# Performance work log

Measured on AMD Instinct MI355X. Metric: run time of the kernel, lower is better.

The kernel has to match this reference:

```python
import jax, jax.numpy as jnp
import numpy as np
from jax import lax
from jax.scipy.special import logsumexp

N, M, K = 50000, 1024, 64          # points, nodes, points-per-patch
D_PT, D_NODE = 64, 256             # point / node feature dims
NUM_CORR = 256                     # coarse correspondences (OT batch)
FINE_TOPK = 3
CONF_TH = 0.05
OUT_CORR = 1024                    # fixed-size fine correspondence output
OT_ITERS = 100
NEG = -1e4                         # finite stand-in for -inf (grad-safe)
EPS = 1e-8


def setup_inputs() -> dict:
    key = jax.random.key(0)
    k = jax.random.split(key, 13)
    f = jnp.float32
    return {
        "src_points": jax.random.uniform(k[0], (N, 3), f) * 10.0,
        "tgt_points": jax.random.uniform(k[1], (N, 3), f) * 10.0,
        "src_point_feats": jax.random.normal(k[2], (N, D_PT), f),
        "tgt_point_feats": jax.random.normal(k[3], (N, D_PT), f),
        "src_node_feats": jax.random.normal(k[4], (M, D_NODE), f),
        "tgt_node_feats": jax.random.normal(k[5], (M, D_NODE), f),
        "src_node_xyz": jax.random.uniform(k[6], (M, 3), f) * 10.0,
        "tgt_node_xyz": jax.random.uniform(k[7], (M, 3), f) * 10.0,
        "coarse_w": jax.random.normal(k[8], (D_NODE, D_NODE), f) / np.sqrt(D_NODE),
        "coarse_b": jnp.zeros((D_NODE,), f),
        "fine_w": jax.random.normal(k[9], (D_NODE, D_PT), f) / np.sqrt(D_PT),
        "fine_b": jnp.zeros((D_NODE,), f),
        "alpha": jnp.ones((), f),
    }


def sq_dist(a, b):
    # squared pairwise distance via gram trick, (Na, Nb)
    return (jnp.sum(a * a, -1)[:, None] + jnp.sum(b * b, -1)[None, :]
            - 2.0 * a @ b.T)


def point_to_node_partition(points, nodes):
    d = sq_dist(points, nodes)                       # (N, M)
    p2n = jnp.argmin(d, axis=1)                      # nearest node per point
    m = nodes.shape[0]
    node_masks = jnp.zeros((m,), bool).at[p2n].set(True)
    match = p2n[:, None] == jnp.arange(m)[None, :]   # point assigned to node
    dm = jnp.where(match, d, 1e12)
    _, knn_idx = lax.top_k(-dm.T, K)                 # (M, K) nearest assigned pts
    knn_node = p2n[knn_idx]
    knn_masks = knn_node == jnp.arange(m)[:, None]
    knn_idx = jnp.where(knn_masks, knn_idx, points.shape[0])  # pad index = N
    return node_masks, knn_idx, knn_masks


def coarse_matching(tgt_feats, src_feats, tgt_masks, src_masks):
    # exp(-||.||^2) similarity + dual normalization (GeoTransformer style)
    scores = jnp.exp(-sq_dist(tgt_feats, src_feats))
    valid = tgt_masks[:, None] & src_masks[None, :]
    scores = jnp.where(valid, scores, 0.0)
    s = (scores / (scores.sum(1, keepdims=True) + EPS)) * \
        (scores / (scores.sum(0, keepdims=True) + EPS))
    vals, idx = lax.top_k(s.reshape(-1), NUM_CORR)
    tgt_idx = idx // src_feats.shape[0]
    src_idx = idx % src_feats.shape[0]
    return tgt_idx, src_idx, vals


def log_optimal_transport(scores, row_masks, col_masks, alpha):
    B, R, C = scores.shape
    pad_c = jnp.broadcast_to(alpha, (B, R, 1)).astype(scores.dtype)
    pad_r = jnp.broadcast_to(alpha, (B, 1, C + 1)).astype(scores.dtype)
    padded = jnp.concatenate([jnp.concatenate([scores, pad_c], 2), pad_r], 1)
    inv_r = jnp.concatenate([~row_masks, jnp.zeros((B, 1), bool)], 1)  # (B,R+1)
    inv_c = jnp.concatenate([~col_masks, jnp.zeros((B, 1), bool)], 1)  # (B,C+1)
    padded = jnp.where(inv_r[:, :, None] | inv_c[:, None, :], NEG, padded)
    nr = row_masks.sum(1).astype(scores.dtype)
    nc = col_masks.sum(1).astype(scores.dtype)
    norm = -jnp.log(nr + nc)
    log_mu = jnp.concatenate(
        [jnp.broadcast_to(norm[:, None], (B, R)), (jnp.log(nc) + norm)[:, None]], 1)
    log_mu = jnp.where(inv_r, NEG, log_mu)
    log_nu = jnp.concatenate(
        [jnp.broadcast_to(norm[:, None], (B, C)), (jnp.log(nr) + norm)[:, None]], 1)
    log_nu = jnp.where(inv_c, NEG, log_nu)

    def body(_, uv):
        u, v = uv
        u = log_mu - logsumexp(padded + v[:, None, :], axis=2)
        v = log_nu - logsumexp(padded + u[:, :, None], axis=1)
        return (u, v)

    u, v = lax.fori_loop(0, OT_ITERS, body,
                         (jnp.zeros_like(log_mu), jnp.zeros_like(log_nu)))
    return padded + u[:, :, None] + v[:, None, :] - norm[:, None, None]


def _topk_row_mask(s, k):
    # boolean mask: True where s is among top-k along the last axis
    idx = lax.top_k(s, k)[1]                          # (B, R, k)
    B, R, _ = s.shape
    b = jnp.arange(B)[:, None, None]
    r = jnp.arange(R)[None, :, None]
    return jnp.zeros(s.shape, bool).at[b, r, idx].set(True)


def fine_matching(tgt_knn_pts, src_knn_pts, tgt_masks, src_masks, ot_scores):
    s = jnp.exp(ot_scores[:, :K, :K])                 # drop dustbin
    mask = tgt_masks[:, :, None] & src_masks[:, None, :]
    rm = _topk_row_mask(s, FINE_TOPK)
    cm = jnp.swapaxes(_topk_row_mask(jnp.swapaxes(s, 1, 2), FINE_TOPK), 1, 2)
    corr = rm & cm & (s > CONF_TH) & mask             # mutual topk + threshold
    sm = jnp.where(corr, s, 0.0)
    vals, idx = lax.top_k(sm.reshape(-1), OUT_CORR)   # fixed-size extraction
    b = idx // (K * K)
    r = (idx // K) % K
    c = idx % K
    valid = vals > 0.0
    tp = jnp.where(valid[:, None], tgt_knn_pts[b, r], 0.0)
    sp = jnp.where(valid[:, None], src_knn_pts[b, c], 0.0)
    return tp, sp, jnp.where(valid, vals, 0.0)


def reference(src_points, tgt_points, src_point_feats, tgt_point_feats,
              src_node_feats, tgt_node_feats, src_node_xyz, tgt_node_xyz,
              coarse_w, coarse_b, fine_w, fine_b, alpha):
    def l2n(x):
        return x / jnp.linalg.norm(x, axis=1, keepdims=True)

    s_node_f = l2n(src_node_feats @ coarse_w.T + coarse_b)
    t_node_f = l2n(tgt_node_feats @ coarse_w.T + coarse_b)
    s_pt_f = src_point_feats @ fine_w.T + fine_b       # (N, 256)
    t_pt_f = tgt_point_feats @ fine_w.T + fine_b

    s_nm, s_knn_i, s_knn_m = point_to_node_partition(src_points, src_node_xyz)
    t_nm, t_knn_i, t_knn_m = point_to_node_partition(tgt_points, tgt_node_xyz)

    s_pad_pts = jnp.concatenate([src_points, jnp.zeros((1, 3), src_points.dtype)], 0)
    t_pad_pts = jnp.concatenate([tgt_points, jnp.zeros((1, 3), tgt_points.dtype)], 0)
    s_knn_pts = s_pad_pts[s_knn_i]                     # (M, K, 3)
    t_knn_pts = t_pad_pts[t_knn_i]

    # coarse matching is under no_grad in the original
    t_ci, s_ci, node_scores = coarse_matching(
        lax.stop_gradient(t_node_f), lax.stop_gradient(s_node_f), t_nm, s_nm)

    s_c_knn_i = s_knn_i[s_ci]; t_c_knn_i = t_knn_i[t_ci]     # (B, K)
    s_c_knn_m = s_knn_m[s_ci]; t_c_knn_m = t_knn_m[t_ci]
    s_c_knn_p = s_knn_pts[s_ci]; t_c_knn_p = t_knn_pts[t_ci]  # (B, K, 3)

    s_pad_f = jnp.concatenate([s_pt_f, jnp.zeros((1, D_NODE), s_pt_f.dtype)], 0)
    t_pad_f = jnp.concatenate([t_pt_f, jnp.zeros((1, D_NODE), t_pt_f.dtype)], 0)
    s_c_knn_f = s_pad_f[s_c_knn_i]                     # (B, K, 256)
    t_c_knn_f = t_pad_f[t_c_knn_i]

    ms = jnp.einsum('bnd,bmd->bnm', t_c_knn_f, s_c_knn_f) / jnp.sqrt(
        jnp.asarray(D_NODE, t_c_knn_f.dtype))
    ms = log_optimal_transport(ms, t_c_knn_m, s_c_knn_m, alpha)  # (B, K+1, K+1)

    tp, sp, cs = fine_matching(lax.stop_gradient(t_c_knn_p),
                               lax.stop_gradient(s_c_knn_p),
                               t_c_knn_m, s_c_knn_m, lax.stop_gradient(ms))
    return ms, tp, sp, cs
```

## Files before the change

### kernel.cpp

```cpp
#include <hip/hip_runtime.h>
#include <math.h>

#define NPTS 50000
#define MN 1024
#define KK 64
#define DPT 64
#define DN 256
#define BCORR 256
#define OUTC 1024
#define OTI 100
#define NEGV (-1e4f)
#define EPSV 1e-8f
#define CAPL 512
#define CCAP 16384
#define HBLK 256
#define RCH 2048

__global__ void zero_all_kernel(int* cnt_s, int* cnt_t, int* ci_t, int* ci_s,
                                float* tpout){
  int t=blockIdx.x*256+threadIdx.x;
  if (t<MN){ cnt_s[t]=0; cnt_t[t]=0; }
  if (t<BCORR){ ci_t[t]=0; ci_s[t]=0; }
  for (int i=t;i<OUTC*3*2+OUTC;i+=gridDim.x*256) tpout[i]=0.0f;
}

__device__ __forceinline__ float blockReduceSum256(float v, float* red){
  int t=threadIdx.x;
  red[t]=v; __syncthreads();
  #pragma unroll
  for (int s=128;s>0;s>>=1){ if(t<s) red[t]+=red[t+s]; __syncthreads(); }
  float r=red[0]; __syncthreads();
  return r;
}

__device__ __forceinline__ void hist_add_agg(unsigned* lh, bool act, unsigned bkt){
  unsigned long long ma=__ballot(act);
  if (ma==0ULL) return;
  unsigned b0=__shfl(bkt, 0, 64);
  unsigned long long m=__ballot(act && bkt==b0);
  int lane=threadIdx.x&63;
  if (m==ma){
    int leader=__ffsll((long long)ma)-1;
    if (act && lane==leader) atomicAdd(&lh[b0],(unsigned)__popcll(ma));
  } else if (act){
    atomicAdd(&lh[bkt],1u);
  }
}

__global__ __launch_bounds__(256) void node_gemm_kernel(
    const float* __restrict__ xt, const float* __restrict__ xs_,
    const float* __restrict__ W, const float* __restrict__ bias,
    float* __restrict__ raw){
  __shared__ float Xs[64][64];
  __shared__ float Ws[64][64];
  int bi=blockIdx.x>>2, bo=blockIdx.x&3;
  const float* x=(bi<16)? xt:xs_;
  int rowbase=(bi&15)*64;
  int t=threadIdx.x, r=t&63, kq=t>>6, tx=t&15, ty=t>>4;
  float acc[4][4]={};
  for (int kc=0;kc<DN;kc+=64){
    __syncthreads();
    const float* xr=x+(size_t)(rowbase+r)*DN+kc+kq*16;
    const float* wr=W+(size_t)(bo*64+r)*DN+kc+kq*16;
    #pragma unroll
    for (int j4=0;j4<4;j4++){
      float4 v=*(const float4*)(xr+4*j4);
      Xs[kq*16+4*j4+0][r]=v.x; Xs[kq*16+4*j4+1][r]=v.y;
      Xs[kq*16+4*j4+2][r]=v.z; Xs[kq*16+4*j4+3][r]=v.w;
      float4 w=*(const float4*)(wr+4*j4);
      Ws[kq*16+4*j4+0][r]=w.x; Ws[kq*16+4*j4+1][r]=w.y;
      Ws[kq*16+4*j4+2][r]=w.z; Ws[kq*16+4*j4+3][r]=w.w;
    }
    __syncthreads();
    #pragma unroll
    for (int kk=0;kk<64;kk++){
      float4 a4=*(const float4*)(&Xs[kk][4*ty]);
      float4 w4=*(const float4*)(&Ws[kk][4*tx]);
      float av[4]={a4.x,a4.y,a4.z,a4.w};
      float wv[4]={w4.x,w4.y,w4.z,w4.w};
      #pragma unroll
      for (int i=0;i<4;i++)
        #pragma unroll
        for (int j=0;j<4;j++) acc[i][j]=fmaf(av[i],wv[j],acc[i][j]);
    }
  }
  size_t gr=(size_t)(bi*64)*DN;
  #pragma unroll
  for (int i=0;i<4;i++){
    int rr=4*ty+i;
    #pragma unroll
    for (int j=0;j<4;j++){
      int oo=4*tx+j;
      raw[gr+(size_t)rr*DN+bo*64+oo]=acc[i][j]+bias[bo*64+oo];
    }
  }
}
__global__ __launch_bounds__(256) void node_norm_kernel(
    const float* __restrict__ raw,
    float* __restrict__ outt, float* __restrict__ outs,
    float* __restrict__ sqt, float* __restrict__ sqs){
  __shared__ float red[256];
  int m=blockIdx.x, i=threadIdx.x;
  float* out=(m<MN)? outt:outs;
  float* sq=(m<MN)? sqt:sqs;
  int mm=(m<MN)? m:m-MN;
  float acc=raw[(size_t)m*DN+i];
  float ssq=blockReduceSum256(acc*acc,red);
  float o=acc/sqrtf(ssq);
  out[mm*DN+i]=o;
  float s2=blockReduceSum256(o*o,red);
  if(i==0) sq[mm]=s2;
}

__global__ __launch_bounds__(256) void p2n_scatter_kernel(
    const float* __restrict__ pts_s, const float* __restrict__ nd_s,
    int* __restrict__ c_s, int* __restrict__ l_s,
    const float* __restrict__ pts_t, const float* __restrict__ nd_t,
    int* __restrict__ c_t, int* __restrict__ l_t,
    int pb){
  __shared__ __align__(16) float4 nd[MN];
  int which=blockIdx.x>=pb;
  const float* pts=which? pts_t:pts_s;
  const float* nodes=which? nd_t:nd_s;
  int* cnt=which? c_t:c_s;
  int* list=which? l_t:l_s;
  int blk=which? blockIdx.x-pb : blockIdx.x;
  for (int j=threadIdx.x;j<MN;j+=256){
    float a=nodes[j*3+0], b=nodes[j*3+1], c=nodes[j*3+2];
    nd[j]=make_float4(a,b,c,a*a+b*b+c*c);
  }
  __syncthreads();
  int id=blk*256+threadIdx.x;
  if (id>=NPTS) return;
  float px=pts[id*3+0], py=pts[id*3+1], pz=pts[id*3+2];
  float pp=px*px+py*py+pz*pz;
  float best=3.4e38f; int bi=0;
  for (int j=0;j<MN;j++){
    float4 n=nd[j];
    float d=pp+n.w-2.0f*(px*n.x+py*n.y+pz*n.z);
    if (d<best){best=d;bi=j;}
  }
  int slot=atomicAdd(&cnt[bi],1);
  if (slot<CAPL) list[(size_t)bi*CAPL+slot]=id;
}

__global__ __launch_bounds__(256) void knn_kernel(
    const float* __restrict__ pts_s, const float* __restrict__ nd_s,
    const int* __restrict__ c_s, const int* __restrict__ l_s, int* __restrict__ k_s,
    const float* __restrict__ pts_t, const float* __restrict__ nd_t,
    const int* __restrict__ c_t, const int* __restrict__ l_t, int* __restrict__ k_t){
  __shared__ float ds[CAPL];
  __shared__ int is[CAPL];
  int which=blockIdx.x>=MN;
  const float* pts=which? pts_t:pts_s;
  const float* nodes=which? nd_t:nd_s;
  const int* cnt=which? c_t:c_s;
  const int* list=which? l_t:l_s;
  int* knn=which? k_t:k_s;
  int m=which? blockIdx.x-MN : blockIdx.x;
  int c=cnt[m]; if (c>CAPL) c=CAPL;
  float ax=nodes[m*3+0], ay=nodes[m*3+1], az=nodes[m*3+2];
  float nn2=ax*ax+ay*ay+az*az;
  for (int e=threadIdx.x;e<c;e+=256){
    int p=list[(size_t)m*CAPL+e];
    float px=pts[p*3+0],py=pts[p*3+1],pz=pts[p*3+2];
    float pp=px*px+py*py+pz*pz;
    ds[e]=pp+nn2-2.0f*(px*ax+py*ay+pz*az);
    is[e]=p;
  }
  for (int k=threadIdx.x;k<KK;k+=256) knn[m*KK+k]=NPTS;
  __syncthreads();
  for (int e=threadIdx.x;e<c;e+=256){
    float d=ds[e]; int p=is[e]; int r=0;
    for (int j=0;j<c;j++){
      float dj=ds[j];
      r += (dj<d || (dj==d && is[j]<p)) ? 1 : 0;
    }
    if (r<KK) knn[m*KK+r]=p;
  }
}

__global__ __launch_bounds__(256) void coarse_score_kernel(
    const float* __restrict__ tf, const float* __restrict__ sf,
    const float* __restrict__ tt, const float* __restrict__ ssv,
    const int* __restrict__ cnt_t, const int* __restrict__ cnt_s, float* __restrict__ S){
  __shared__ float tas[64][64];
  __shared__ float sbs[64][64];
  __shared__ float tta[64], ssa[64], tva[64], sva[64];
  int bi=blockIdx.x>>4, bj=blockIdx.x&15;
  int t=threadIdx.x, r=t&63, kq=t>>6, tx=t&15, ty=t>>4;
  if (kq==0){ tta[r]=tt[bi*64+r]; tva[r]=(cnt_t[bi*64+r]>0)?1.f:0.f; }
  if (kq==1){ ssa[r]=ssv[bj*64+r]; sva[r]=(cnt_s[bj*64+r]>0)?1.f:0.f; }
  float acc[4][4]={};
  const float* ta=tf+((size_t)bi*64)*DN;
  const float* sa=sf+((size_t)bj*64)*DN;
  for (int kc=0;kc<DN;kc+=64){
    __syncthreads();
    const float* tr_=ta+(size_t)r*DN+kc+kq*16;
    const float* sr_=sa+(size_t)r*DN+kc+kq*16;
    #pragma unroll
    for (int j4=0;j4<4;j4++){
      float4 v=*(const float4*)(tr_+4*j4);
      tas[kq*16+4*j4+0][r]=v.x; tas[kq*16+4*j4+1][r]=v.y;
      tas[kq*16+4*j4+2][r]=v.z; tas[kq*16+4*j4+3][r]=v.w;
      float4 w=*(const float4*)(sr_+4*j4);
      sbs[kq*16+4*j4+0][r]=w.x; sbs[kq*16+4*j4+1][r]=w.y;
      sbs[kq*16+4*j4+2][r]=w.z; sbs[kq*16+4*j4+3][r]=w.w;
    }
    __syncthreads();
    #pragma unroll
    for (int kk=0;kk<64;kk++){
      float4 a4=*(const float4*)(&tas[kk][4*ty]);
      float4 b4=*(const float4*)(&sbs[kk][4*tx]);
      float av[4]={a4.x,a4.y,a4.z,a4.w};
      float bv[4]={b4.x,b4.y,b4.z,b4.w};
      #pragma unroll
      for (int i=0;i<4;i++)
        #pragma unroll
        for (int j=0;j<4;j++) acc[i][j]=fmaf(av[i],bv[j],acc[i][j]);
    }
  }
  __syncthreads();
  #pragma unroll
  for (int i=0;i<4;i++){
    int rr=4*ty+i;
    #pragma unroll
    for (int j=0;j<4;j++){
      int cc=4*tx+j;
      float d=tta[rr]+ssa[cc]-2.0f*acc[i][j];
      float v=expf(-d);
      S[(size_t)(bi*64+rr)*MN + bj*64+cc]=(tva[rr]>0.f && sva[cc]>0.f)? v:0.0f;
    }
  }
}

__global__ __launch_bounds__(256) void sums_kernel(
    const float* __restrict__ S, float* __restrict__ rs, float* __restrict__ cs){
  __shared__ float red[256];
  __shared__ float red2[16][17];
  if (blockIdx.x<MN){
    int i=blockIdx.x;
    float a=0;
    for (int j=threadIdx.x;j<MN;j+=256) a+=S[(size_t)i*MN+j];
    float r=blockReduceSum256(a,red);
    if (threadIdx.x==0) rs[i]=r;
  } else {
    int j0=(blockIdx.x-MN)*16;
    int tx=threadIdx.x&15, ty=threadIdx.x>>4;
    float a=0;
    for (int i=ty;i<MN;i+=16) a+=S[(size_t)i*MN + j0+tx];
    red2[ty][tx]=a; __syncthreads();
    if (ty==0){
      float s=0;
      #pragma unroll
      for (int q=0;q<16;q++) s+=red2[q][tx];
      cs[j0+tx]=s;
    }
  }
}
__global__ __launch_bounds__(256) void dualnorm_hist_kernel(
    float* __restrict__ S, const float* __restrict__ rs, const float* __restrict__ cs,
    unsigned* __restrict__ partial1){
  __shared__ unsigned lh[256];
  lh[threadIdx.x]=0u; __syncthreads();
  for (int idx=blockIdx.x*256+threadIdx.x; idx<MN*MN; idx+=gridDim.x*256){
    int i=idx>>10, j=idx&1023;
    float v=S[idx];
    v=(v/(rs[i]+EPSV))*(v/(cs[j]+EPSV));
    S[idx]=v;
    bool act=(v>0.0f);
    unsigned bkt=act? (__float_as_uint(v)>>24) : 0xFFFFFFFFu;
    hist_add_agg(lh,act,bkt);
  }
  __syncthreads();
  partial1[blockIdx.x*256+threadIdx.x]=lh[threadIdx.x];
}

__device__ __forceinline__ int scan_top(const unsigned* h, int k, unsigned start,
                                        unsigned* outcum){
  unsigned cum=start;
  for (int b=255;b>=0;b--){
    if (cum+h[b] >= (unsigned)k){ *outcum=cum; return b; }
    cum+=h[b];
  }
  *outcum=cum;
  return -1;
}
__device__ __forceinline__ void sum_partials(const unsigned* __restrict__ p,
                                             unsigned* h, int t){
  unsigned a=0;
  for (int i=0;i<HBLK;i++) a+=p[(size_t)i*256+t];
  h[t]=a;
}

__global__ __launch_bounds__(256) void hist_fine_kernel(
    const float* __restrict__ arr, int n, int k,
    const unsigned* __restrict__ p1, unsigned* __restrict__ p2){
  __shared__ unsigned h[256];
  __shared__ unsigned lh[256];
  __shared__ unsigned cbS;
  int t=threadIdx.x;
  lh[t]=0u;
  sum_partials(p1,h,t);
  __syncthreads();
  if (t==0){
    unsigned ab; int cb=scan_top(h,k,0u,&ab);
    if (cb<0) cb=0;
    cbS=(unsigned)cb;
  }
  __syncthreads();
  unsigned CB=cbS;
  for (int i=blockIdx.x*256+t; i<n; i+=gridDim.x*256){
    float v=arr[i];
    unsigned b=__float_as_uint(v);
    bool act=(v>0.0f && (b>>24)==CB);
    hist_add_agg(lh,act,(b>>16)&255u);
  }
  __syncthreads();
  p2[blockIdx.x*256+t]=lh[t];
}
__global__ __launch_bounds__(256) void hist_fine2_kernel(
    const float* __restrict__ arr, int n, int k,
    const unsigned* __restrict__ p1, const unsigned* __restrict__ p2,
    unsigned* __restrict__ p3, unsigned* __restrict__ cnt){
  __shared__ unsigned h[256];
  __shared__ unsigned lh[256];
  __shared__ unsigned t16S;
  int t=threadIdx.x;
  if (blockIdx.x==0 && t==0) *cnt=0u;
  lh[t]=0u;
  sum_partials(p1,h,t);
  __syncthreads();
  __shared__ unsigned cbS, ab1S;
  if (t==0){
    unsigned ab; int cb=scan_top(h,k,0u,&ab);
    if (cb<0){ cb=0; ab=ab-h[0]; }
    cbS=(unsigned)cb; ab1S=ab;
  }
  __syncthreads();
  sum_partials(p2,h,t);
  __syncthreads();
  if (t==0){
    unsigned ab2; int sb=scan_top(h,k,ab1S,&ab2);
    if (sb<0) sb=0;
    t16S=cbS*256u+(unsigned)sb;
  }
  __syncthreads();
  unsigned T16=t16S;
  for (int i=blockIdx.x*256+t; i<n; i+=gridDim.x*256){
    float v=arr[i];
    unsigned b=__float_as_uint(v);
    bool act=(v>0.0f && (b>>16)==T16);
    hist_add_agg(lh,act,(b>>8)&255u);
  }
  __syncthreads();
  p3[blockIdx.x*256+t]=lh[t];
}
__global__ __launch_bounds__(256) void compact_kernel(
    const float* __restrict__ arr, int n, int k,
    const unsigned* __restrict__ p1, const unsigned* __restrict__ p2,
    const unsigned* __restrict__ p3,
    float* __restrict__ cv, int* __restrict__ ci, unsigned* __restrict__ cnt){
  __shared__ unsigned h[256];
  __shared__ unsigned cbS, ab1S, t16S, ab2S, t24S;
  int t=threadIdx.x;
  sum_partials(p1,h,t);
  __syncthreads();
  if (t==0){
    unsigned ab; int cb=scan_top(h,k,0u,&ab);
    if (cb<0){ cb=0; ab=ab-h[0]; }
    cbS=(unsigned)cb; ab1S=ab;
  }
  __syncthreads();
  sum_partials(p2,h,t);
  __syncthreads();
  if (t==0){
    unsigned ab2; int sb=scan_top(h,k,ab1S,&ab2);
    if (sb<0) sb=0;
    t16S=cbS*256u+(unsigned)sb; ab2S=ab2;
  }
  __syncthreads();
  sum_partials(p3,h,t);
  __syncthreads();
  if (t==0){
    unsigned ab3; int sb=scan_top(h,k,ab2S,&ab3);
    if (sb<0) sb=0;
    t24S=t16S*256u+(unsigned)sb;
  }
  __syncthreads();
  unsigned T=t24S;
  for (int i=blockIdx.x*256+t; i<n; i+=gridDim.x*256){
    float v=arr[i];
    if (v>0.0f && (__float_as_uint(v)>>8)>=T){
      unsigned p=atomicAdd(cnt,1u);
      if (p<CCAP){ cv[p]=v; ci[p]=i; }
    }
  }
}
__global__ __launch_bounds__(256) void rank_coarse_kernel(
    const float* __restrict__ cv, const int* __restrict__ ci, const unsigned* __restrict__ meta,
    int* __restrict__ ti, int* __restrict__ si){
  __shared__ __align__(16) float scv[RCH];
  __shared__ __align__(16) int sci[RCH];
  int c=(int)meta[1]; if (c>CCAP) c=CCAP;
  int t=blockIdx.x*256+threadIdx.x;
  bool act=(t<c);
  float v=0.0f; int idx=0;
  if (act){ v=cv[t]; idx=ci[t]; }
  int rk=0;
  for (int base=0;base<c;base+=RCH){
    int lim=min(RCH,c-base);
    __syncthreads();
    for (int j=threadIdx.x;j<lim;j+=256){ scv[j]=cv[base+j]; sci[j]=ci[base+j]; }
    __syncthreads();
    if (act){
      int j=0;
      for (;j+4<=lim;j+=4){
        float4 v4=*(const float4*)(scv+j);
        int4 i4=*(const int4*)(sci+j);
        rk += (v4.x>v||(v4.x==v&&i4.x<idx))?1:0;
        rk += (v4.y>v||(v4.y==v&&i4.y<idx))?1:0;
        rk += (v4.z>v||(v4.z==v&&i4.z<idx))?1:0;
        rk += (v4.w>v||(v4.w==v&&i4.w<idx))?1:0;
      }
      for (;j<lim;j++) rk += (scv[j]>v||(scv[j]==v&&sci[j]<idx))?1:0;
    }
  }
  if (act && rk<BCORR){ ti[rk]=idx/MN; si[rk]=idx%MN; }
}
__global__ __launch_bounds__(256) void rank_fine_kernel(
    const float* __restrict__ cv, const int* __restrict__ ci, const unsigned* __restrict__ meta,
    const int* __restrict__ sel_t, const int* __restrict__ sel_s,
    const float* __restrict__ tpts, const float* __restrict__ spts,
    float* __restrict__ tp, float* __restrict__ sp, float* __restrict__ cs){
  __shared__ __align__(16) float scv[RCH];
  __shared__ __align__(16) int sci[RCH];
  int c=(int)meta[1]; if (c>CCAP) c=CCAP;
  int t=blockIdx.x*256+threadIdx.x;
  bool act=(t<c);
  float v=0.0f; int idx=0;
  if (act){ v=cv[t]; idx=ci[t]; }
  int rk=0;
  for (int base=0;base<c;base+=RCH){
    int lim=min(RCH,c-base);
    __syncthreads();
    for (int j=threadIdx.x;j<lim;j+=256){ scv[j]=cv[base+j]; sci[j]=ci[base+j]; }
    __syncthreads();
    if (act){
      int j=0;
      for (;j+4<=lim;j+=4){
        float4 v4=*(const float4*)(scv+j);
        int4 i4=*(const int4*)(sci+j);
        rk += (v4.x>v||(v4.x==v&&i4.x<idx))?1:0;
        rk += (v4.y>v||(v4.y==v&&i4.y<idx))?1:0;
        rk += (v4.z>v||(v4.z==v&&i4.z<idx))?1:0;
        rk += (v4.w>v||(v4.w==v&&i4.w<idx))?1:0;
      }
      for (;j<lim;j++) rk += (scv[j]>v||(scv[j]==v&&sci[j]<idx))?1:0;
    }
  }
  if (act && rk<OUTC){
    int b=idx>>12, r=(idx>>6)&63, cc=idx&63;
    int tpi=sel_t[b*KK+r], spi=sel_s[b*KK+cc];
    float tx=0,ty=0,tz=0,sx=0,sy=0,sz=0;
    if (tpi<NPTS){ tx=tpts[tpi*3]; ty=tpts[tpi*3+1]; tz=tpts[tpi*3+2]; }
    if (spi<NPTS){ sx=spts[spi*3]; sy=spts[spi*3+1]; sz=spts[spi*3+2]; }
    tp[rk*3+0]=tx; tp[rk*3+1]=ty; tp[rk*3+2]=tz;
    sp[rk*3+0]=sx; sp[rk*3+1]=sy; sp[rk*3+2]=sz;
    cs[rk]=v;
  }
}

__global__ __launch_bounds__(256) void sel_feat_kernel(
    const int* __restrict__ ci_t, const int* __restrict__ knn_t, const float* __restrict__ ptf_t,
    const int* __restrict__ ci_s, const int* __restrict__ knn_s, const float* __restrict__ ptf_s,
    const float* __restrict__ W, const float* __restrict__ bias,
    float* __restrict__ out_t, float* __restrict__ out_s,
    int* __restrict__ sel_tO, int* __restrict__ sel_sO){
  __shared__ float Xs[64][64];
  __shared__ float Ws[64][64];
  __shared__ float pvf[64];
  int which=blockIdx.x>=1024;
  const int* cib=which? ci_s:ci_t;
  const int* knn=which? knn_s:knn_t;
  const float* ptf=which? ptf_s:ptf_t;
  float* out=which? out_s:out_t;
  int* sel=which? sel_sO:sel_tO;
  int blk=which? blockIdx.x-1024 : blockIdx.x;
  int bj=blk>>2, bo=blk&3;
  int t=threadIdx.x, r=t&63, kq=t>>6, tx=t&15, ty=t>>4;
  int p=knn[cib[bj]*KK+r];
  if (kq==0){
    pvf[r]=(p!=NPTS)?1.f:0.f;
    if (bo==0) sel[bj*KK+r]=p;
  }
  const float* xr=ptf+(size_t)p*DPT+kq*16;
  #pragma unroll
  for (int j4=0;j4<4;j4++){
    float4 v=(p==NPTS)? make_float4(0.f,0.f,0.f,0.f) : *(const float4*)(xr+4*j4);
    Xs[kq*16+4*j4+0][r]=v.x; Xs[kq*16+4*j4+1][r]=v.y;
    Xs[kq*16+4*j4+2][r]=v.z; Xs[kq*16+4*j4+3][r]=v.w;
  }
  const float* wr=W+(size_t)(bo*64+r)*DPT+kq*16;
  #pragma unroll
  for (int j4=0;j4<4;j4++){
    float4 w=*(const float4*)(wr+4*j4);
    Ws[kq*16+4*j4+0][r]=w.x; Ws[kq*16+4*j4+1][r]=w.y;
    Ws[kq*16+4*j4+2][r]=w.z; Ws[kq*16+4*j4+3][r]=w.w;
  }
  __syncthreads();
  float acc[4][4]={};
  #pragma unroll
  for (int kk=0;kk<64;kk++){
    float4 a4=*(const float4*)(&Xs[kk][4*ty]);
    float4 w4=*(const float4*)(&Ws[kk][4*tx]);
    float av[4]={a4.x,a4.y,a4.z,a4.w};
    float wv[4]={w4.x,w4.y,w4.z,w4.w};
    #pragma unroll
    for (int i=0;i<4;i++)
      #pragma unroll
      for (int j=0;j<4;j++) acc[i][j]=fmaf(av[i],wv[j],acc[i][j]);
  }
  #pragma unroll
  for (int i=0;i<4;i++){
    int rr=4*ty+i;
    #pragma unroll
    for (int j=0;j<4;j++){
      int oo=4*tx+j;
      float v=acc[i][j]+bias[bo*64+oo];
      out[(size_t)(bj*64+rr)*DN + bo*64+oo]= (pvf[rr]>0.f)? v : 0.0f;
    }
  }
}

__global__ __launch_bounds__(256) void pbuild_kernel(
    const float* __restrict__ ft, const float* __restrict__ fs,
    const int* __restrict__ sel_t, const int* __restrict__ sel_s,
    const float* __restrict__ alpha_p, float* __restrict__ P){
  __shared__ float tas[64][64];
  __shared__ float sbs[64][64];
  __shared__ float tmv[64], smv[64];
  int b=blockIdx.x, t=threadIdx.x;
  int r=t&63, kq=t>>6, tx=t&15, ty=t>>4;
  if (kq==0) tmv[r]=(sel_t[b*KK+r]!=NPTS)?1.f:0.f;
  if (kq==1) smv[r]=(sel_s[b*KK+r]!=NPTS)?1.f:0.f;
  float acc[4][4]={};
  const float* tb=ft+(size_t)b*KK*DN;
  const float* sb=fs+(size_t)b*KK*DN;
  for (int kc=0;kc<DN;kc+=64){
    __syncthreads();
    const float* tr_=tb+(size_t)r*DN+kc+kq*16;
    const float* sr_=sb+(size_t)r*DN+kc+kq*16;
    #pragma unroll
    for (int j4=0;j4<4;j4++){
      float4 v=*(const float4*)(tr_+4*j4);
      tas[kq*16+4*j4+0][r]=v.x; tas[kq*16+4*j4+1][r]=v.y;
      tas[kq*16+4*j4+2][r]=v.z; tas[kq*16+4*j4+3][r]=v.w;
      float4 w=*(const float4*)(sr_+4*j4);
      sbs[kq*16+4*j4+0][r]=w.x; sbs[kq*16+4*j4+1][r]=w.y;
      sbs[kq*16+4*j4+2][r]=w.z; sbs[kq*16+4*j4+3][r]=w.w;
    }
    __syncthreads();
    #pragma unroll
    for (int kk=0;kk<64;kk++){
      float4 a4=*(const float4*)(&tas[kk][4*ty]);
      float4 b4=*(const float4*)(&sbs[kk][4*tx]);
      float av[4]={a4.x,a4.y,a4.z,a4.w};
      float bv[4]={b4.x,b4.y,b4.z,b4.w};
      #pragma unroll
      for (int i=0;i<4;i++)
        #pragma unroll
        for (int j=0;j<4;j++) acc[i][j]=fmaf(av[i],bv[j],acc[i][j]);
    }
  }
  __syncthreads();
  float alpha=alpha_p[0];
  float* Pb=P+(size_t)b*65*65;
  #pragma unroll
  for (int i=0;i<4;i++){
    int rr=4*ty+i;
    bool tok=tmv[rr]>0.f;
    #pragma unroll
    for (int j=0;j<4;j++){
      int cc=4*tx+j;
      bool invm=(!tok)||(smv[cc]<=0.f);
      Pb[rr*65+cc]= invm ? NEGV : acc[i][j]*0.0625f;
    }
  }
  if (t<64){
    Pb[64*65+t]=(smv[t]<=0.f)? NEGV : alpha;
    Pb[t*65+64]=(tmv[t]<=0.f)? NEGV : alpha;
  }
  if (t==64) Pb[64*65+64]=alpha;
}

__global__ __launch_bounds__(256,1) void ot_kernel(
    float* __restrict__ P, const int* __restrict__ sel_t, const int* __restrict__ sel_s){
  __shared__ float Ps[4225];
  __shared__ __align__(16) float partU[4][72], partV[4][72];
  __shared__ __align__(16) float pu64[4], pusv[4], pv64[4], pvsv[4];
  __shared__ float ufs[65], vfs[65];
  int b=blockIdx.x, t=threadIdx.x, w=t>>6, l=t&63;
  float* Pg=P+(size_t)b*4225;
  for (int e=t;e<4225;e+=256) Ps[e]=Pg[e];
  bool rv=(sel_t[b*KK+l]!=NPTS);
  bool cv=(sel_s[b*KK+l]!=NPTS);
  int nr=(int)__popcll(__ballot(rv));
  int nc=(int)__popcll(__ballot(cv));
  float inv=1.0f/(float)(nr+nc);
  float nrm=-logf((float)(nr+nc));
  float mu_l=inv, nu_l=inv, mu64=(float)nc*inv, nu64=(float)nr*inv;
  bool anyInvR=(nr<KK), anyInvC=(nc<KK);
  __syncthreads();
  const int c0=16*w;
  float aQ[16], bQ[16], r64Q[16], c64Q[16];
  #pragma unroll
  for (int j=0;j<16;j++){
    aQ[j]  =expf(Ps[l*65+c0+j]);
    bQ[j]  =expf(Ps[(c0+j)*65+l]);
    r64Q[j]=expf(Ps[64*65+c0+j]);
    c64Q[j]=expf(Ps[(c0+j)*65+64]);
  }
  float a64=expf(Ps[l*65+64]);
  float b64v=expf(Ps[64*65+l]);
  float k6464=expf(Ps[4224]);
  float U_l, V_l=1.0f, U64, V64=1.0f;

  for (int it=0; it<OTI; ++it){
    float p0=0,p1f=0,p2f=0,p3=0, d0=0,d1=0,d2=0,d3=0, z0=0,z1=0,z2=0,z3=0;
    #pragma unroll
    for (int j4=0;j4<4;j4++){
      float v0=__int_as_float(__builtin_amdgcn_readlane(__float_as_int(V_l), c0+4*j4+0));
      float v1=__int_as_float(__builtin_amdgcn_readlane(__float_as_int(V_l), c0+4*j4+1));
      float v2=__int_as_float(__builtin_amdgcn_readlane(__float_as_int(V_l), c0+4*j4+2));
      float v3=__int_as_float(__builtin_amdgcn_readlane(__float_as_int(V_l), c0+4*j4+3));
      p0=fmaf(aQ[4*j4+0],v0,p0); p1f=fmaf(aQ[4*j4+1],v1,p1f);
      p2f=fmaf(aQ[4*j4+2],v2,p2f); p3=fmaf(aQ[4*j4+3],v3,p3);
      d0=fmaf(r64Q[4*j4+0],v0,d0); d1=fmaf(r64Q[4*j4+1],v1,d1);
      d2=fmaf(r64Q[4*j4+2],v2,d2); d3=fmaf(r64Q[4*j4+3],v3,d3);
      z0+=v0; z1+=v1; z2+=v2; z3+=v3;
    }
    partU[w][l]=(p0+p1f)+(p2f+p3);
    if (l==0){ pu64[w]=(d0+d1)+(d2+d3); pusv[w]=(z0+z1)+(z2+z3); }
    __syncthreads();
    {
      float s=partU[0][l]+partU[1][l]+partU[2][l]+partU[3][l];
      float4 d4=*(const float4*)pu64;
      float srow=s+a64*V64;
      float s64=(d4.x+d4.y)+(d4.z+d4.w)+k6464*V64;
      U64=mu64/s64;
      if (anyInvR){
        float4 z4=*(const float4*)pusv;
        float sv=(z4.x+z4.y)+(z4.z+z4.w)+V64;
        U_l = rv ? (mu_l/srow) : (1.0f/sv);
      } else U_l = mu_l/srow;
    }
    float q0=0,q1=0,q2=0,q3=0, e0=0,e1=0,e2=0,e3=0, y0=0,y1=0,y2=0,y3=0;
    #pragma unroll
    for (int j4=0;j4<4;j4++){
      float u0=__int_as_float(__builtin_amdgcn_readlane(__float_as_int(U_l), c0+4*j4+0));
      float u1=__int_as_float(__builtin_amdgcn_readlane(__float_as_int(U_l), c0+4*j4+1));
      float u2=__int_as_float(__builtin_amdgcn_readlane(__float_as_int(U_l), c0+4*j4+2));
      float u3=__int_as_float(__builtin_amdgcn_readlane(__float_as_int(U_l), c0+4*j4+3));
      q0=fmaf(bQ[4*j4+0],u0,q0); q1=fmaf(bQ[4*j4+1],u1,q1);
      q2=fmaf(bQ[4*j4+2],u2,q2); q3=fmaf(bQ[4*j4+3],u3,q3);
      e0=fmaf(c64Q[4*j4+0],u0,e0); e1=fmaf(c64Q[4*j4+1],u1,e1);
      e2=fmaf(c64Q[4*j4+2],u2,e2); e3=fmaf(c64Q[4*j4+3],u3,e3);
      y0+=u0; y1+=u1; y2+=u2; y3+=u3;
    }
    partV[w][l]=(q0+q1)+(q2+q3);
    if (l==0){ pv64[w]=(e0+e1)+(e2+e3); pvsv[w]=(y0+y1)+(y2+y3); }
    __syncthreads();
    {
      float sc=partV[0][l]+partV[1][l]+partV[2][l]+partV[3][l];
      float4 e4=*(const float4*)pv64;
      float scol=sc+b64v*U64;
      float s64v=(e4.x+e4.y)+(e4.z+e4.w)+k6464*U64;
      V64=nu64/s64v;
      if (anyInvC){
        float4 y4=*(const float4*)pvsv;
        float su=(y4.x+y4.y)+(y4.z+y4.w)+U64;
        V_l = cv ? (nu_l/scol) : (1.0f/su);
      } else V_l = nu_l/scol;
    }
  }
  if (w==0){
    ufs[l]=logf(U_l); vfs[l]=logf(V_l);
    if (l==0){ ufs[64]=logf(U64); vfs[64]=logf(V64); }
  }
  __syncthreads();
  for (int e=t;e<4225;e+=256){
    int r=e/65, c=e-65*r;
    Pg[e]=Ps[e]+ufs[r]+vfs[c]-nrm;
  }
}

__global__ __launch_bounds__(256) void fineprep_kernel(
    const float* __restrict__ P, const int* __restrict__ sel_t, const int* __restrict__ sel_s,
    float* __restrict__ smout, unsigned* __restrict__ partial1){
  __shared__ float s[KK*KK];
  __shared__ unsigned long long rowm[KK], colm[KK];
  __shared__ int tmk[KK], smk[KK];
  __shared__ unsigned lh[256];
  int b=blockIdx.x, t=threadIdx.x;
  lh[t]=0u;
  const float* Pb=P+(size_t)b*65*65;
  for (int e=t;e<KK*KK;e+=256){
    int r=e>>6, c=e&63;
    s[e]=expf(Pb[r*65+c]);
  }
  if (t<KK){ tmk[t]=(sel_t[b*KK+t]!=NPTS); smk[t]=(sel_s[b*KK+t]!=NPTS); }
  __syncthreads();
  if (t<KK){
    float v1=-1,v2=-1,v3=-1; int i1=0,i2=0,i3=0;
    const float* row=s+t*KK;
    for (int c=0;c<KK;c++){ float v=row[c];
      if (v>v1){v3=v2;i3=i2;v2=v1;i2=i1;v1=v;i1=c;}
      else if (v>v2){v3=v2;i3=i2;v2=v;i2=c;}
      else if (v>v3){v3=v;i3=c;}
    }
    rowm[t]=(1ULL<<i1)|(1ULL<<i2)|(1ULL<<i3);
  } else if (t<2*KK){
    int c=t-KK;
    float v1=-1,v2=-1,v3=-1; int i1=0,i2=0,i3=0;
    for (int r=0;r<KK;r++){ float v=s[r*KK+c];
      if (v>v1){v3=v2;i3=i2;v2=v1;i2=i1;v1=v;i1=r;}
      else if (v>v2){v3=v2;i3=i2;v2=v;i2=r;}
      else if (v>v3){v3=v;i3=r;}
    }
    colm[c]=(1ULL<<i1)|(1ULL<<i2)|(1ULL<<i3);
  }
  __syncthreads();
  for (int e=t;e<KK*KK;e+=256){
    int r=e>>6, c=e&63;
    float v=s[e];
    bool keep = ((rowm[r]>>c)&1ULL) && ((colm[c]>>r)&1ULL) && (v>0.05f) && tmk[r] && smk[c];
    float o= keep? v : 0.0f;
    smout[(size_t)b*KK*KK+e]=o;
    if (o>0.0f) atomicAdd(&lh[__float_as_uint(o)>>24],1u);
  }
  __syncthreads();
  partial1[b*256+t]=lh[t];
}

extern "C" void kernel_launch(void* const* d_in, const int* in_sizes, int n_in,
                              void* d_out, int out_size, void* d_ws, size_t ws_size,
                              hipStream_t stream){
  const float* src_pts=(const float*)d_in[0];
  const float* tgt_pts=(const float*)d_in[1];
  const float* src_pf =(const float*)d_in[2];
  const float* tgt_pf =(const float*)d_in[3];
  const float* src_nf =(const float*)d_in[4];
  const float* tgt_nf =(const float*)d_in[5];
  const float* src_nx =(const float*)d_in[6];
  const float* tgt_nx =(const float*)d_in[7];
  const float* cw=(const float*)d_in[8];
  const float* cb=(const float*)d_in[9];
  const float* fw=(const float*)d_in[10];
  const float* fb=(const float*)d_in[11];
  const float* alpha=(const float*)d_in[12];

  char* ws=(char*)d_ws;
  size_t off=0;
  auto A=[&](size_t bytes)->char*{
    char* p=ws+off; off+=(bytes+255)&~(size_t)255; return p; };

  float* tf    =(float*)A((size_t)MN*DN*4);
  float* sfb   =(float*)A((size_t)MN*DN*4);
  float* nfr   =(float*)A((size_t)2*MN*DN*4);
  float* tt    =(float*)A(MN*4);
  float* ssv   =(float*)A(MN*4);
  int*   cnt_s =(int*)A(MN*4);
  int*   cnt_t =(int*)A(MN*4);
  int*   list_s=(int*)A((size_t)MN*CAPL*4);
  int*   list_t=(int*)A((size_t)MN*CAPL*4);
  int*   knn_s =(int*)A((size_t)MN*KK*4);
  int*   knn_t =(int*)A((size_t)MN*KK*4);
  float* Smat  =(float*)A((size_t)MN*MN*4);
  unsigned* partial1=(unsigned*)A((size_t)HBLK*256*4);
  unsigned* partial2=(unsigned*)A((size_t)HBLK*256*4);
  unsigned* partial3=(unsigned*)A((size_t)HBLK*256*4);
  unsigned* meta=(unsigned*)A(256);
  float* cand_v=(float*)A((size_t)CCAP*4);
  int*   cand_i=(int*)A((size_t)CCAP*4);
  int*   ci_t  =(int*)A(BCORR*4);
  int*   ci_s  =(int*)A(BCORR*4);
  int*   sel_t =(int*)A((size_t)BCORR*KK*4);
  int*   sel_s =(int*)A((size_t)BCORR*KK*4);
  float* feat_t=(float*)A((size_t)BCORR*KK*DN*4);
  float* feat_s=(float*)A((size_t)BCORR*KK*DN*4);
  float* smf   =(float*)A((size_t)BCORR*KK*KK*4);
  float* rs    =(float*)A(MN*4);
  float* csum  =(float*)A(MN*4);

  float* out=(float*)d_out;
  float* msout=out;
  float* tpout=out+(size_t)BCORR*65*65;
  float* spout=tpout+(size_t)OUTC*3;
  float* csout=spout+(size_t)OUTC*3;

  const int PB=(NPTS+255)/256;

  zero_all_kernel<<<28,256,0,stream>>>(cnt_s,cnt_t,ci_t,ci_s,tpout);
  node_gemm_kernel<<<128,256,0,stream>>>(tgt_nf,src_nf,cw,cb,nfr);
  node_norm_kernel<<<2*MN,256,0,stream>>>(nfr,tf,sfb,tt,ssv);
  p2n_scatter_kernel<<<2*PB,256,0,stream>>>(src_pts,src_nx,cnt_s,list_s,
                                            tgt_pts,tgt_nx,cnt_t,list_t,PB);
  knn_kernel<<<2*MN,256,0,stream>>>(src_pts,src_nx,cnt_s,list_s,knn_s,
                                    tgt_pts,tgt_nx,cnt_t,list_t,knn_t);

  coarse_score_kernel<<<256,256,0,stream>>>(tf,sfb,tt,ssv,cnt_t,cnt_s,Smat);
  sums_kernel<<<MN+64,256,0,stream>>>(Smat,rs,csum);
  dualnorm_hist_kernel<<<HBLK,256,0,stream>>>(Smat,rs,csum,partial1);

  hist_fine_kernel<<<HBLK,256,0,stream>>>(Smat,MN*MN,BCORR,partial1,partial2);
  hist_fine2_kernel<<<HBLK,256,0,stream>>>(Smat,MN*MN,BCORR,partial1,partial2,partial3,meta+1);
  compact_kernel<<<256,256,0,stream>>>(Smat,MN*MN,BCORR,partial1,partial2,partial3,
                                       cand_v,cand_i,meta+1);
  rank_coarse_kernel<<<CCAP/256,256,0,stream>>>(cand_v,cand_i,meta,ci_t,ci_s);

  sel_feat_kernel<<<2048,256,0,stream>>>(ci_t,knn_t,tgt_pf, ci_s,knn_s,src_pf,
                                         fw,fb,feat_t,feat_s,sel_t,sel_s);

  pbuild_kernel<<<BCORR,256,0,stream>>>(feat_t,feat_s,sel_t,sel_s,alpha,msout);
  ot_kernel<<<BCORR,256,0,stream>>>(msout,sel_t,sel_s);

  fineprep_kernel<<<BCORR,256,0,stream>>>(msout,sel_t,sel_s,smf,partial1);
  hist_fine_kernel<<<HBLK,256,0,stream>>>(smf,BCORR*KK*KK,OUTC,partial1,partial2);
  hist_fine2_kernel<<<HBLK,256,0,stream>>>(smf,BCORR*KK*KK,OUTC,partial1,partial2,partial3,meta+1);
  compact_kernel<<<256,256,0,stream>>>(smf,BCORR*KK*KK,OUTC,partial1,partial2,partial3,
                                       cand_v,cand_i,meta+1);
  rank_fine_kernel<<<CCAP/256,256,0,stream>>>(cand_v,cand_i,meta,sel_t,sel_s,
                                              tgt_pts,src_pts,tpout,spout,csout);
}
```

Measured before the change: 530.2 us.

## Fuse radix-select histogram, compact and rank stages into one cooperative kernel

Result: slower. 644.6 us (+21.6%).

```diff
diff --git a/kernel.cpp b/kernel.cpp
--- a/kernel.cpp
+++ b/kernel.cpp
@@ -1,5 +1,8 @@
 #include <hip/hip_runtime.h>
+#include <hip/hip_cooperative_groups.h>
 #include <math.h>
+
+namespace cg = cooperative_groups;
 
 #define NPTS 50000
 #define MN 1024
@@ -293,20 +296,29 @@
   h[t]=a;
 }
 
-__global__ __launch_bounds__(256) void hist_fine_kernel(
-    const float* __restrict__ arr, int n, int k,
-    const unsigned* __restrict__ p1, unsigned* __restrict__ p2){
+__global__ __launch_bounds__(256) void select_kernel(
+    const float* __restrict__ arr, int n, int k, int mode,
+    const unsigned* __restrict__ p1, unsigned* __restrict__ p2,
+    unsigned* __restrict__ p3, unsigned* __restrict__ meta,
+    float* __restrict__ cv, int* __restrict__ ci,
+    int* __restrict__ ti, int* __restrict__ si,
+    const int* __restrict__ sel_t, const int* __restrict__ sel_s,
+    const float* __restrict__ tpts, const float* __restrict__ spts,
+    float* __restrict__ tp, float* __restrict__ sp, float* __restrict__ cso){
+  cg::grid_group grid=cg::this_grid();
   __shared__ unsigned h[256];
   __shared__ unsigned lh[256];
-  __shared__ unsigned cbS;
+  __shared__ unsigned cbS, ab1S, t16S, ab2S, t24S;
+  __shared__ __align__(16) float scv[RCH];
+  __shared__ __align__(16) int sci[RCH];
   int t=threadIdx.x;
   lh[t]=0u;
   sum_partials(p1,h,t);
   __syncthreads();
   if (t==0){
     unsigned ab; int cb=scan_top(h,k,0u,&ab);
-    if (cb<0) cb=0;
-    cbS=(unsigned)cb;
+    if (cb<0){ cb=0; ab=ab-h[0]; }
+    cbS=(unsigned)cb; ab1S=ab;
   }
   __syncthreads();
   unsigned CB=cbS;
@@ -318,32 +330,15 @@
   }
   __syncthreads();
   p2[blockIdx.x*256+t]=lh[t];
-}
-__global__ __launch_bounds__(256) void hist_fine2_kernel(
-    const float* __restrict__ arr, int n, int k,
-    const unsigned* __restrict__ p1, const unsigned* __restrict__ p2,
-    unsigned* __restrict__ p3, unsigned* __restrict__ cnt){
-  __shared__ unsigned h[256];
-  __shared__ unsigned lh[256];
-  __shared__ unsigned t16S;
-  int t=threadIdx.x;
-  if (blockIdx.x==0 && t==0) *cnt=0u;
+  grid.sync();
   lh[t]=0u;
-  sum_partials(p1,h,t);
-  __syncthreads();
-  __shared__ unsigned cbS, ab1S;
-  if (t==0){
-    unsigned ab; int cb=scan_top(h,k,0u,&ab);
-    if (cb<0){ cb=0; ab=ab-h[0]; }
-    cbS=(unsigned)cb; ab1S=ab;
-  }
-  __syncthreads();
+  if (blockIdx.x==0 && t==0) meta[1]=0u;
   sum_partials(p2,h,t);
   __syncthreads();
   if (t==0){
     unsigned ab2; int sb=scan_top(h,k,ab1S,&ab2);
     if (sb<0) sb=0;
-    t16S=cbS*256u+(unsigned)sb;
+    t16S=cbS*256u+(unsigned)sb; ab2S=ab2;
   }
   __syncthreads();
   unsigned T16=t16S;
@@ -355,31 +350,7 @@
   }
   __syncthreads();
   p3[blockIdx.x*256+t]=lh[t];
-}
-__global__ __launch_bounds__(256) void compact_kernel(
-    const float* __restrict__ arr, int n, int k,
-    const unsigned* __restrict__ p1, const unsigned* __restrict__ p2,
-    const unsigned* __restrict__ p3,
-    float* __restrict__ cv, int* __restrict__ ci, unsigned* __restrict__ cnt){
-  __shared__ unsigned h[256];
-  __shared__ unsigned cbS, ab1S, t16S, ab2S, t24S;
-  int t=threadIdx.x;
-  sum_partials(p1,h,t);
-  __syncthreads();
-  if (t==0){
-    unsigned ab; int cb=scan_top(h,k,0u,&ab);
-    if (cb<0){ cb=0; ab=ab-h[0]; }
-    cbS=(unsigned)cb; ab1S=ab;
-  }
-  __syncthreads();
-  sum_partials(p2,h,t);
-  __syncthreads();
-  if (t==0){
-    unsigned ab2; int sb=scan_top(h,k,ab1S,&ab2);
-    if (sb<0) sb=0;
-    t16S=cbS*256u+(unsigned)sb; ab2S=ab2;
-  }
-  __syncthreads();
+  grid.sync();
   sum_partials(p3,h,t);
   __syncthreads();
   if (t==0){
@@ -392,26 +363,21 @@
   for (int i=blockIdx.x*256+t; i<n; i+=gridDim.x*256){
     float v=arr[i];
     if (v>0.0f && (__float_as_uint(v)>>8)>=T){
-      unsigned p=atomicAdd(cnt,1u);
+      unsigned p=atomicAdd(&meta[1],1u);
       if (p<CCAP){ cv[p]=v; ci[p]=i; }
     }
   }
-}
-__global__ __launch_bounds__(256) void rank_coarse_kernel(
-    const float* __restrict__ cv, const int* __restrict__ ci, const unsigned* __restrict__ meta,
-    int* __restrict__ ti, int* __restrict__ si){
-  __shared__ __align__(16) float scv[RCH];
-  __shared__ __align__(16) int sci[RCH];
+  grid.sync();
   int c=(int)meta[1]; if (c>CCAP) c=CCAP;
-  int t=blockIdx.x*256+threadIdx.x;
-  bool act=(t<c);
+  int gt=blockIdx.x*256+t;
+  bool act=(gt<c);
   float v=0.0f; int idx=0;
-  if (act){ v=cv[t]; idx=ci[t]; }
+  if (act){ v=cv[gt]; idx=ci[gt]; }
   int rk=0;
   for (int base=0;base<c;base+=RCH){
     int lim=min(RCH,c-base);
     __syncthreads();
-    for (int j=threadIdx.x;j<lim;j+=256){ scv[j]=cv[base+j]; sci[j]=ci[base+j]; }
+    for (int j=t;j<lim;j+=256){ scv[j]=cv[base+j]; sci[j]=ci[base+j]; }
     __syncthreads();
     if (act){
       int j=0;
@@ -426,48 +392,21 @@
       for (;j<lim;j++) rk += (scv[j]>v||(scv[j]==v&&sci[j]<idx))?1:0;
     }
   }
-  if (act && rk<BCORR){ ti[rk]=idx/MN; si[rk]=idx%MN; }
-}
-__global__ __launch_bounds__(256) void rank_fine_kernel(
-    const float* __restrict__ cv, const int* __restrict__ ci, const unsigned* __restrict__ meta,
-    const int* __restrict__ sel_t, const int* __restrict__ sel_s,
-    const float* __restrict__ tpts, const float* __restrict__ spts,
-    float* __restrict__ tp, float* __restrict__ sp, float* __restrict__ cs){
-  __shared__ __align__(16) float scv[RCH];
-  __shared__ __align__(16) int sci[RCH];
-  int c=(int)meta[1]; if (c>CCAP) c=CCAP;
-  int t=blockIdx.x*256+threadIdx.x;
-  bool act=(t<c);
-  float v=0.0f; int idx=0;
-  if (act){ v=cv[t]; idx=ci[t]; }
-  int rk=0;
-  for (int base=0;base<c;base+=RCH){
-    int lim=min(RCH,c-base);
-    __syncthreads();
-    for (int j=threadIdx.x;j<lim;j+=256){ scv[j]=cv[base+j]; sci[j]=ci[base+j]; }
-    __syncthreads();
-    if (act){
-      int j=0;
-      for (;j+4<=lim;j+=4){
-        float4 v4=*(const float4*)(scv+j);
-        int4 i4=*(const int4*)(sci+j);
-        rk += (v4.x>v||(v4.x==v&&i4.x<idx))?1:0;
-        rk += (v4.y>v||(v4.y==v&&i4.y<idx))?1:0;
-        rk += (v4.z>v||(v4.z==v&&i4.z<idx))?1:0;
-        rk += (v4.w>v||(v4.w==v&&i4.w<idx))?1:0;
+  if (act){
+    if (mode==0){
+      if (rk<BCORR){ ti[rk]=idx/MN; si[rk]=idx%MN; }
+    } else {
+      if (rk<OUTC){
+        int b=idx>>12, r=(idx>>6)&63, cc=idx&63;
+        int tpi=sel_t[b*KK+r], spi=sel_s[b*KK+cc];
+        float tx=0,ty=0,tz=0,sx=0,sy=0,sz=0;
+        if (tpi<NPTS){ tx=tpts[tpi*3]; ty=tpts[tpi*3+1]; tz=tpts[tpi*3+2]; }
+        if (spi<NPTS){ sx=spts[spi*3]; sy=spts[spi*3+1]; sz=spts[spi*3+2]; }
+        tp[rk*3+0]=tx; tp[rk*3+1]=ty; tp[rk*3+2]=tz;
+        sp[rk*3+0]=sx; sp[rk*3+1]=sy; sp[rk*3+2]=sz;
+        cso[rk]=v;
       }
-      for (;j<lim;j++) rk += (scv[j]>v||(scv[j]==v&&sci[j]<idx))?1:0;
-    }
-  }
-  if (act && rk<OUTC){
-    int b=idx>>12, r=(idx>>6)&63, cc=idx&63;
-    int tpi=sel_t[b*KK+r], spi=sel_s[b*KK+cc];
-    float tx=0,ty=0,tz=0,sx=0,sy=0,sz=0;
-    if (tpi<NPTS){ tx=tpts[tpi*3]; ty=tpts[tpi*3+1]; tz=tpts[tpi*3+2]; }
-    if (spi<NPTS){ sx=spts[spi*3]; sy=spts[spi*3+1]; sz=spts[spi*3+2]; }
-    tp[rk*3+0]=tx; tp[rk*3+1]=ty; tp[rk*3+2]=tz;
-    sp[rk*3+0]=sx; sp[rk*3+1]=sy; sp[rk*3+2]=sz;
-    cs[rk]=v;
+    }
   }
 }
 
@@ -813,11 +752,19 @@
   sums_kernel<<<MN+64,256,0,stream>>>(Smat,rs,csum);
   dualnorm_hist_kernel<<<HBLK,256,0,stream>>>(Smat,rs,csum,partial1);
 
-  hist_fine_kernel<<<HBLK,256,0,stream>>>(Smat,MN*MN,BCORR,partial1,partial2);
-  hist_fine2_kernel<<<HBLK,256,0,stream>>>(Smat,MN*MN,BCORR,partial1,partial2,partial3,meta+1);
-  compact_kernel<<<256,256,0,stream>>>(Smat,MN*MN,BCORR,partial1,partial2,partial3,
-                                       cand_v,cand_i,meta+1);
-  rank_coarse_kernel<<<CCAP/256,256,0,stream>>>(cand_v,cand_i,meta,ci_t,ci_s);
+  {
+    const float* arrC=Smat; int nC=MN*MN; int kC=BCORR; int modeC=0;
+    const unsigned* p1C=partial1; unsigned* p2C=partial2; unsigned* p3C=partial3;
+    unsigned* metaC=meta; float* cvC=cand_v; int* ciC=cand_i;
+    int* tiC=ci_t; int* siC=ci_s;
+    const int* seltC=sel_t; const int* selsC=sel_s;
+    const float* tpc=tgt_pts; const float* spc=src_pts;
+    float* tpo=tpout; float* spo=spout; float* cso=csout;
+    void* args[]={&arrC,&nC,&kC,&modeC,&p1C,&p2C,&p3C,&metaC,&cvC,&ciC,
+                  &tiC,&siC,&seltC,&selsC,&tpc,&spc,&tpo,&spo,&cso};
+    hipLaunchCooperativeKernel((const void*)select_kernel,dim3(256),dim3(256),
+                               args,0,stream);
+  }
 
   sel_feat_kernel<<<2048,256,0,stream>>>(ci_t,knn_t,tgt_pf, ci_s,knn_s,src_pf,
                                          fw,fb,feat_t,feat_s,sel_t,sel_s);
@@ -826,10 +773,18 @@
   ot_kernel<<<BCORR,256,0,stream>>>(msout,sel_t,sel_s);
 
   fineprep_kernel<<<BCORR,256,0,stream>>>(msout,sel_t,sel_s,smf,partial1);
-  hist_fine_kernel<<<HBLK,256,0,stream>>>(smf,BCORR*KK*KK,OUTC,partial1,partial2);
-  hist_fine2_kernel<<<HBLK,256,0,stream>>>(smf,BCORR*KK*KK,OUTC,partial1,partial2,partial3,meta+1);
-  compact_kernel<<<256,256,0,stream>>>(smf,BCORR*KK*KK,OUTC,partial1,partial2,partial3,
-                                       cand_v,cand_i,meta+1);
-  rank_fine_kernel<<<CCAP/256,256,0,stream>>>(cand_v,cand_i,meta,sel_t,sel_s,
-                                              tgt_pts,src_pts,tpout,spout,csout);
-}
+
+  {
+    const float* arrF=smf; int nF=BCORR*KK*KK; int kF=OUTC; int modeF=1;
+    const unsigned* p1F=partial1; unsigned* p2F=partial2; unsigned* p3F=partial3;
+    unsigned* metaF=meta; float* cvF=cand_v; int* ciF=cand_i;
+    int* tiF=ci_t; int* siF=ci_s;
+    const int* seltF=sel_t; const int* selsF=sel_s;
+    const float* tpf2=tgt_pts; const float* spf2=src_pts;
+    float* tpo=tpout; float* spo=spout; float* cso=csout;
+    void* args[]={&arrF,&nF,&kF,&modeF,&p1F,&p2F,&p3F,&metaF,&cvF,&ciF,
+                  &tiF,&siF,&seltF,&selsF,&tpf2,&spf2,&tpo,&spo,&cso};
+    hipLaunchCooperativeKernel((const void*)select_kernel,dim3(256),dim3(256),
+                               args,0,stream);
+  }
+}
```
